# Kernel tuning notes

Hardware: AMD Instinct MI355X
Metric: run time of the kernel (lower is better)

## Reference

```python
import jax, jax.numpy as jnp
import numpy as np

N_NODES = 50000
N_EDGES = 800000
DIM = 128
LN_EPS = 1e-5


def _gcn_conv(x, src, dst, W, b, n_nodes):
    h = x @ W  # [N, D]
    loop = jnp.arange(n_nodes, dtype=src.dtype)
    src_f = jnp.concatenate([src, loop])
    dst_f = jnp.concatenate([dst, loop])
    deg = jax.ops.segment_sum(jnp.ones_like(dst_f, dtype=h.dtype), dst_f,
                              num_segments=n_nodes)  # in-degree incl. self-loop (>=1)
    dinv = jax.lax.rsqrt(deg)
    norm = dinv[src_f] * dinv[dst_f]  # [E+N]
    msg = norm[:, None] * h[src_f]  # gather + scale
    out = jax.ops.segment_sum(msg, dst_f, num_segments=n_nodes)
    return out + b


def _layer_norm(h, w, b):
    mu = jnp.mean(h, axis=-1, keepdims=True)
    var = jnp.mean(jnp.square(h - mu), axis=-1, keepdims=True)
    return (h - mu) * jax.lax.rsqrt(var + LN_EPS) * w + b


def setup_inputs() -> dict:
    key = jax.random.key(0)
    ks = jax.random.split(key, 8)
    x = jax.random.normal(ks[0], (N_NODES, DIM), dtype=jnp.float32)
    edge_index = jax.random.randint(ks[1], (2, N_EDGES), 0, N_NODES, dtype=jnp.int64)
    s = 1.0 / np.sqrt(DIM)
    W0 = jax.random.uniform(ks[2], (DIM, DIM), jnp.float32, -s, s)
    b0 = jnp.zeros((DIM,), jnp.float32)
    W1 = jax.random.uniform(ks[3], (DIM, DIM), jnp.float32, -s, s)
    b1 = jnp.zeros((DIM,), jnp.float32)
    ln0_w = jnp.ones((DIM,), jnp.float32)
    ln0_b = jnp.zeros((DIM,), jnp.float32)
    ln1_w = jnp.ones((DIM,), jnp.float32)
    ln1_b = jnp.zeros((DIM,), jnp.float32)
    return {"x": x, "edge_index": edge_index, "W0": W0, "b0": b0, "W1": W1,
            "b1": b1, "ln0_w": ln0_w, "ln0_b": ln0_b, "ln1_w": ln1_w, "ln1_b": ln1_b}


def reference(x, edge_index, W0, b0, W1, b1, ln0_w, ln0_b, ln1_w, ln1_b):
    src, dst = edge_index[0], edge_index[1]
    n = x.shape[0]
    # layer 0 (dropout is identity in eval mode)
    h = _gcn_conv(x, src, dst, W0, b0, n)
    h = jax.nn.relu(_layer_norm(h, ln0_w, ln0_b)) + x
    # layer 1
    h2 = _gcn_conv(h, src, dst, W1, b1, n)
    h2 = jax.nn.relu(_layer_norm(h2, ln1_w, ln1_b)) + h
    return h2
```

## Files before the change

kernel.cpp:

```cpp
#include <hip/hip_runtime.h>
#include <hip/hip_bf16.h>

#define NDIM 128
#define NNODES 50000
#define CAP 64
#define SWZ(b) ((b) ^ ((((b) >> 8) & 7) << 4))

typedef short bf16x8 __attribute__((ext_vector_type(8)));
typedef float f32x4 __attribute__((ext_vector_type(4)));

__device__ __forceinline__ unsigned short f2bf(float f) {
    unsigned u = __builtin_bit_cast(unsigned, f);
    unsigned r = (u + 0x7FFF + ((u >> 16) & 1)) >> 16;
    return (unsigned short)r;
}
__device__ __forceinline__ float bf2f(unsigned short u) {
    return __builtin_bit_cast(float, (unsigned)u << 16);
}

__device__ __forceinline__ void gl_lds16(const void* g, void* l) {
    __builtin_amdgcn_global_load_lds(
        (const __attribute__((address_space(1))) unsigned int*)g,
        (__attribute__((address_space(3))) unsigned int*)l, 16, 0, 0);
}

__global__ __launch_bounds__(256) void k_build(const int* __restrict__ src,
                                               const int* __restrict__ dst,
                                               int* __restrict__ cnt,
                                               int* __restrict__ bucket, int E) {
    int e = blockIdx.x * 256 + threadIdx.x;
    if (e >= E) return;
    int d = dst[e];
    int p = atomicAdd(&cnt[d], 1);
    if (p < CAP) bucket[(long)d * CAP + p] = src[e];
}

__global__ __launch_bounds__(256) void k_prep(const int* __restrict__ cnt,
                                              float* __restrict__ dinv,
                                              const float* __restrict__ W0,
                                              const float* __restrict__ W1,
                                              unsigned short* __restrict__ Ws0,
                                              unsigned short* __restrict__ Ws1) {
    int b = blockIdx.x;
    if (b < 196) {
        int i = b * 256 + threadIdx.x;
        if (i < NNODES) dinv[i] = rsqrtf((float)cnt[i] + 1.0f);
    } else {
        int t = (b - 196) * 256 + threadIdx.x;
        const float* W = (t >> 14) ? W1 : W0;
        unsigned short* Wd = (t >> 14) ? Ws1 : Ws0;
        int e = t & 16383;
        int k = e >> 7, c = e & 127;
        int byteb = c * 256 + k * 2;
        Wd[SWZ(byteb) >> 1] = f2bf(W[k * NDIM + c]);
    }
}

__global__ __launch_bounds__(256) void k_gemm(const float* __restrict__ X,
                                              const unsigned short* __restrict__ Wsw,
                                              const float* __restrict__ dinv,
                                              unsigned short* __restrict__ Hb,
                                              int n) {
    __shared__ char sW[32768];
    const int wave = threadIdx.x >> 6, lane = threadIdx.x & 63;
    {
        const char* g = (const char*)Wsw;
#pragma unroll
        for (int i = 0; i < 8; i++) {
            int off = (i * 4 + wave) * 1024 + lane * 16;
            gl_lds16(g + off, sW + off);
        }
    }
    const int r16 = lane & 15, hi = lane >> 4;
    const int nodeb = blockIdx.x * 64 + wave * 16;
    int arow = nodeb + r16; if (arow > n - 1) arow = n - 1;

    bf16x8 a[4];
    const float* xp = X + (size_t)arow * NDIM + hi * 8;
#pragma unroll
    for (int kc = 0; kc < 4; kc++) {
        float4 f0 = *(const float4*)(xp + kc * 32);
        float4 f1 = *(const float4*)(xp + kc * 32 + 4);
        bf16x8 v;
        v[0] = f2bf(f0.x); v[1] = f2bf(f0.y); v[2] = f2bf(f0.z); v[3] = f2bf(f0.w);
        v[4] = f2bf(f1.x); v[5] = f2bf(f1.y); v[6] = f2bf(f1.z); v[7] = f2bf(f1.w);
        a[kc] = v;
    }
    float dr[4];
#pragma unroll
    for (int r = 0; r < 4; r++) {
        int row = nodeb + hi * 4 + r;
        dr[r] = dinv[row < n ? row : n - 1];
    }
    __syncthreads();

#pragma unroll
    for (int ct = 0; ct < 8; ct++) {
        f32x4 acc = {0.f, 0.f, 0.f, 0.f};
#pragma unroll
        for (int kc = 0; kc < 4; kc++) {
            int bb = (ct * 16 + r16) * 256 + kc * 64 + hi * 16;
            bf16x8 bw = *(const bf16x8*)(sW + SWZ(bb));
            acc = __builtin_amdgcn_mfma_f32_16x16x32_bf16(a[kc], bw, acc, 0, 0, 0);
        }
#pragma unroll
        for (int r = 0; r < 4; r++) {
            int row = nodeb + hi * 4 + r;
            if (row < n)
                Hb[(size_t)row * NDIM + ct * 16 + r16] = f2bf(acc[r] * dr[r]);
        }
    }
}

__global__ __launch_bounds__(256) void k_agg(const unsigned short* __restrict__ hb,
                                             const float* __restrict__ xres,
                                             const int* __restrict__ bucket,
                                             const int* __restrict__ cnt,
                                             const float* __restrict__ dinv,
                                             const float* __restrict__ bias,
                                             const float* __restrict__ lnw,
                                             const float* __restrict__ lnb,
                                             float* __restrict__ out) {
    const int tid = threadIdx.x;
    const int l16 = tid & 15;
    const int node = blockIdx.x * 16 + (tid >> 4);
    const int d0 = l16 * 8;

    const float dv = dinv[node];
    int c = cnt[node]; if (c > CAP) c = CAP;

    float acc[8];
    {
        bf16x8 sv = *(const bf16x8*)(hb + (size_t)node * NDIM + d0);
#pragma unroll
        for (int t = 0; t < 8; t++) acc[t] = bf2f((unsigned short)sv[t]);
    }

    const int* bk = bucket + (size_t)node * CAP;
    int j = 0;
    for (; j + 4 <= c; j += 4) {
        int s0 = bk[j], s1 = bk[j + 1], s2 = bk[j + 2], s3 = bk[j + 3];
        bf16x8 r0 = *(const bf16x8*)(hb + (size_t)s0 * NDIM + d0);
        bf16x8 r1 = *(const bf16x8*)(hb + (size_t)s1 * NDIM + d0);
        bf16x8 r2 = *(const bf16x8*)(hb + (size_t)s2 * NDIM + d0);
        bf16x8 r3 = *(const bf16x8*)(hb + (size_t)s3 * NDIM + d0);
#pragma unroll
        for (int t = 0; t < 8; t++)
            acc[t] += (bf2f((unsigned short)r0[t]) + bf2f((unsigned short)r1[t]))
                    + (bf2f((unsigned short)r2[t]) + bf2f((unsigned short)r3[t]));
    }
    for (; j < c; j++) {
        int s = bk[j];
        bf16x8 r = *(const bf16x8*)(hb + (size_t)s * NDIM + d0);
#pragma unroll
        for (int t = 0; t < 8; t++) acc[t] += bf2f((unsigned short)r[t]);
    }

    float v[8];
    float4 bb0 = *(const float4*)(bias + d0);
    float4 bb1 = *(const float4*)(bias + d0 + 4);
    v[0] = fmaf(dv, acc[0], bb0.x); v[1] = fmaf(dv, acc[1], bb0.y);
    v[2] = fmaf(dv, acc[2], bb0.z); v[3] = fmaf(dv, acc[3], bb0.w);
    v[4] = fmaf(dv, acc[4], bb1.x); v[5] = fmaf(dv, acc[5], bb1.y);
    v[6] = fmaf(dv, acc[6], bb1.z); v[7] = fmaf(dv, acc[7], bb1.w);

    float s = 0.f;
#pragma unroll
    for (int t = 0; t < 8; t++) s += v[t];
#pragma unroll
    for (int o = 1; o < 16; o <<= 1) s += __shfl_xor(s, o);
    const float mu = s * (1.0f / 128.0f);

    float e[8], q = 0.f;
#pragma unroll
    for (int t = 0; t < 8; t++) { e[t] = v[t] - mu; q += e[t] * e[t]; }
#pragma unroll
    for (int o = 1; o < 16; o <<= 1) q += __shfl_xor(q, o);
    const float rinv = rsqrtf(q * (1.0f / 128.0f) + 1e-5f);

    float4 w0 = *(const float4*)(lnw + d0), w1 = *(const float4*)(lnw + d0 + 4);
    float4 lb0 = *(const float4*)(lnb + d0), lb1 = *(const float4*)(lnb + d0 + 4);
    float4 x0 = *(const float4*)(xres + (size_t)node * NDIM + d0);
    float4 x1 = *(const float4*)(xres + (size_t)node * NDIM + d0 + 4);

    float4 o0, o1;
    o0.x = fmaxf(fmaf(e[0] * rinv, w0.x, lb0.x), 0.f) + x0.x;
    o0.y = fmaxf(fmaf(e[1] * rinv, w0.y, lb0.y), 0.f) + x0.y;
    o0.z = fmaxf(fmaf(e[2] * rinv, w0.z, lb0.z), 0.f) + x0.z;
    o0.w = fmaxf(fmaf(e[3] * rinv, w0.w, lb0.w), 0.f) + x0.w;
    o1.x = fmaxf(fmaf(e[4] * rinv, w1.x, lb1.x), 0.f) + x1.x;
    o1.y = fmaxf(fmaf(e[5] * rinv, w1.y, lb1.y), 0.f) + x1.y;
    o1.z = fmaxf(fmaf(e[6] * rinv, w1.z, lb1.z), 0.f) + x1.z;
    o1.w = fmaxf(fmaf(e[7] * rinv, w1.w, lb1.w), 0.f) + x1.w;
    *(float4*)(out + (size_t)node * NDIM + d0) = o0;
    *(float4*)(out + (size_t)node * NDIM + d0 + 4) = o1;
}

extern "C" void kernel_launch(void* const* d_in, const int* in_sizes, int n_in,
                              void* d_out, int out_size, void* d_ws, size_t ws_size,
                              hipStream_t stream) {
    const float* x    = (const float*)d_in[0];
    const int*   ei   = (const int*)d_in[1];
    const float* W0   = (const float*)d_in[2];
    const float* b0   = (const float*)d_in[3];
    const float* W1   = (const float*)d_in[4];
    const float* b1   = (const float*)d_in[5];
    const float* ln0w = (const float*)d_in[6];
    const float* ln0b = (const float*)d_in[7];
    const float* ln1w = (const float*)d_in[8];
    const float* ln1b = (const float*)d_in[9];
    float* out = (float*)d_out;

    const int E = in_sizes[1] / 2;
    const int* src = ei;
    const int* dst = ei + E;

    char* ws = (char*)d_ws;
    size_t o = 0;
    int*   cnt    = (int*)(ws + o);                 o += (size_t)50048 * 4;
    float* dinv   = (float*)(ws + o);               o += (size_t)50048 * 4;
    int*   bucket = (int*)(ws + o);                 o += (size_t)NNODES * CAP * 4;
    unsigned short* hb = (unsigned short*)(ws + o); o += (size_t)NNODES * NDIM * 2;
    float* xmid   = (float*)(ws + o);               o += (size_t)NNODES * NDIM * 4;
    unsigned short* Ws0 = (unsigned short*)(ws + o); o += (size_t)NDIM * NDIM * 2;
    unsigned short* Ws1 = (unsigned short*)(ws + o); o += (size_t)NDIM * NDIM * 2;

    hipMemsetAsync(cnt, 0, NNODES * sizeof(int), stream);
    k_build<<<(E + 255) / 256, 256, 0, stream>>>(src, dst, cnt, bucket, E);
    k_prep<<<324, 256, 0, stream>>>(cnt, dinv, W0, W1, Ws0, Ws1);

    const int gemm_grid = (NNODES + 63) / 64;
    k_gemm<<<gemm_grid, 256, 0, stream>>>(x, Ws0, dinv, hb, NNODES);
    k_agg<<<NNODES / 16, 256, 0, stream>>>(hb, x, bucket, cnt, dinv, b0,
                                           ln0w, ln0b, xmid);
    k_gemm<<<gemm_grid, 256, 0, stream>>>(xmid, Ws1, dinv, hb, NNODES);
    k_agg<<<NNODES / 16, 256, 0, stream>>>(hb, xmid, bucket, cnt, dinv, b1,
                                           ln1w, ln1b, out);
}
```

Measured before the change: 229.6 us.

## Overlap CSR bucket build with first GEMM in a combined kernel

Merges the edge-bucket build into the first GEMM launch: extra blocks beyond the GEMM grid run the atomic bucket fill while the other blocks compute X·W0. Because the degrees are not known yet, the GEMM writes unscaled bf16 rows, and a new k_scale pass computes dinv and rescales hb afterward. The aim is to hide the atomic-heavy build behind the GEMM and remove one launch. The cost is an extra read-modify-write pass over hb and a second bf16 rounding of the scaled values. Bucket stores also become nontemporal.

```diff
diff --git a/kernel.cpp b/kernel.cpp
--- a/kernel.cpp
+++ b/kernel.cpp
@@ -5,6 +5,8 @@
 #define NNODES 50000
 #define CAP 64
 #define SWZ(b) ((b) ^ ((((b) >> 8) & 7) << 4))
+#define GEMM_GRID 782
+#define BUILD_GRID 2048
 
 typedef short bf16x8 __attribute__((ext_vector_type(8)));
 typedef float f32x4 __attribute__((ext_vector_type(4)));
@@ -24,36 +26,97 @@
         (__attribute__((address_space(3))) unsigned int*)l, 16, 0, 0);
 }
 
-__global__ __launch_bounds__(256) void k_build(const int* __restrict__ src,
-                                               const int* __restrict__ dst,
-                                               int* __restrict__ cnt,
-                                               int* __restrict__ bucket, int E) {
-    int e = blockIdx.x * 256 + threadIdx.x;
-    if (e >= E) return;
-    int d = dst[e];
-    int p = atomicAdd(&cnt[d], 1);
-    if (p < CAP) bucket[(long)d * CAP + p] = src[e];
-}
-
-__global__ __launch_bounds__(256) void k_prep(const int* __restrict__ cnt,
-                                              float* __restrict__ dinv,
-                                              const float* __restrict__ W0,
+__global__ __launch_bounds__(256) void k_prep(const float* __restrict__ W0,
                                               const float* __restrict__ W1,
                                               unsigned short* __restrict__ Ws0,
                                               unsigned short* __restrict__ Ws1) {
-    int b = blockIdx.x;
-    if (b < 196) {
-        int i = b * 256 + threadIdx.x;
-        if (i < NNODES) dinv[i] = rsqrtf((float)cnt[i] + 1.0f);
-    } else {
-        int t = (b - 196) * 256 + threadIdx.x;
-        const float* W = (t >> 14) ? W1 : W0;
-        unsigned short* Wd = (t >> 14) ? Ws1 : Ws0;
-        int e = t & 16383;
-        int k = e >> 7, c = e & 127;
-        int byteb = c * 256 + k * 2;
-        Wd[SWZ(byteb) >> 1] = f2bf(W[k * NDIM + c]);
-    }
+    int t = blockIdx.x * 256 + threadIdx.x;
+    const float* W = (t >> 14) ? W1 : W0;
+    unsigned short* Wd = (t >> 14) ? Ws1 : Ws0;
+    int e = t & 16383;
+    int k = e >> 7, c = e & 127;
+    int byteb = c * 256 + k * 2;
+    Wd[SWZ(byteb) >> 1] = f2bf(W[k * NDIM + c]);
+}
+
+__global__ __launch_bounds__(256) void k_mega(const float* __restrict__ X,
+                                              const unsigned short* __restrict__ Wsw,
+                                              unsigned short* __restrict__ Hb,
+                                              const int* __restrict__ src,
+                                              const int* __restrict__ dst,
+                                              int* __restrict__ cnt,
+                                              int* __restrict__ bucket,
+                                              int E, int n) {
+    __shared__ char sW[32768];
+    if (blockIdx.x >= GEMM_GRID) {
+        int e0 = (blockIdx.x - GEMM_GRID) * 256 + threadIdx.x;
+        for (int e = e0; e < E; e += BUILD_GRID * 256) {
+            int d = dst[e];
+            int p = atomicAdd(&cnt[d], 1);
+            if (p < CAP)
+                __builtin_nontemporal_store(src[e], &bucket[(long)d * CAP + p]);
+        }
+        return;
+    }
+    const int wave = threadIdx.x >> 6, lane = threadIdx.x & 63;
+    {
+        const char* g = (const char*)Wsw;
+#pragma unroll
+        for (int i = 0; i < 8; i++) {
+            int off = (i * 4 + wave) * 1024 + lane * 16;
+            gl_lds16(g + off, sW + off);
+        }
+    }
+    const int r16 = lane & 15, hi = lane >> 4;
+    const int nodeb = blockIdx.x * 64 + wave * 16;
+    int arow = nodeb + r16; if (arow > n - 1) arow = n - 1;
+
+    bf16x8 a[4];
+    const float* xp = X + (size_t)arow * NDIM + hi * 8;
+#pragma unroll
+    for (int kc = 0; kc < 4; kc++) {
+        float4 f0 = *(const float4*)(xp + kc * 32);
+        float4 f1 = *(const float4*)(xp + kc * 32 + 4);
+        bf16x8 v;
+        v[0] = f2bf(f0.x); v[1] = f2bf(f0.y); v[2] = f2bf(f0.z); v[3] = f2bf(f0.w);
+        v[4] = f2bf(f1.x); v[5] = f2bf(f1.y); v[6] = f2bf(f1.z); v[7] = f2bf(f1.w);
+        a[kc] = v;
+    }
+    __syncthreads();
+
+#pragma unroll
+    for (int ct = 0; ct < 8; ct++) {
+        f32x4 acc = {0.f, 0.f, 0.f, 0.f};
+#pragma unroll
+        for (int kc = 0; kc < 4; kc++) {
+            int bb = (ct * 16 + r16) * 256 + kc * 64 + hi * 16;
+            bf16x8 bw = *(const bf16x8*)(sW + SWZ(bb));
+            acc = __builtin_amdgcn_mfma_f32_16x16x32_bf16(a[kc], bw, acc, 0, 0, 0);
+        }
+#pragma unroll
+        for (int r = 0; r < 4; r++) {
+            int row = nodeb + hi * 4 + r;
+            if (row < n)
+                Hb[(size_t)row * NDIM + ct * 16 + r16] = f2bf(acc[r]);
+        }
+    }
+}
+
+__global__ __launch_bounds__(256) void k_scale(unsigned short* __restrict__ hb,
+                                               const int* __restrict__ cnt,
+                                               float* __restrict__ dinv) {
+    const int tid = threadIdx.x;
+    const int l16 = tid & 15;
+    const int row = blockIdx.x * 16 + (tid >> 4);
+    const float dv = rsqrtf((float)cnt[row] + 1.0f);
+    if (l16 == 0) dinv[row] = dv;
+    unsigned short* p = hb + (size_t)row * NDIM + l16 * 8;
+    bf16x8 v = *(const bf16x8*)p;
+    bf16x8 o;
+#pragma unroll
+    for (int t = 0; t < 8; t++)
+        o[t] = (short)f2bf(bf2f((unsigned short)v[t]) * dv);
+    *(bf16x8*)p = o;
 }
 
 __global__ __launch_bounds__(256) void k_gemm(const float* __restrict__ X,
@@ -217,23 +280,23 @@
 
     char* ws = (char*)d_ws;
     size_t o = 0;
-    int*   cnt    = (int*)(ws + o);                 o += (size_t)50048 * 4;
-    float* dinv   = (float*)(ws + o);               o += (size_t)50048 * 4;
-    int*   bucket = (int*)(ws + o);                 o += (size_t)NNODES * CAP * 4;
-    unsigned short* hb = (unsigned short*)(ws + o); o += (size_t)NNODES * NDIM * 2;
-    float* xmid   = (float*)(ws + o);               o += (size_t)NNODES * NDIM * 4;
+    int*   cnt    = (int*)(ws + o);                  o += (size_t)50048 * 4;
+    float* dinv   = (float*)(ws + o);                o += (size_t)50048 * 4;
+    int*   bucket = (int*)(ws + o);                  o += (size_t)NNODES * CAP * 4;
+    unsigned short* hb = (unsigned short*)(ws + o);  o += (size_t)NNODES * NDIM * 2;
+    float* xmid   = (float*)(ws + o);                o += (size_t)NNODES * NDIM * 4;
     unsigned short* Ws0 = (unsigned short*)(ws + o); o += (size_t)NDIM * NDIM * 2;
     unsigned short* Ws1 = (unsigned short*)(ws + o); o += (size_t)NDIM * NDIM * 2;
 
     hipMemsetAsync(cnt, 0, NNODES * sizeof(int), stream);
-    k_build<<<(E + 255) / 256, 256, 0, stream>>>(src, dst, cnt, bucket, E);
-    k_prep<<<324, 256, 0, stream>>>(cnt, dinv, W0, W1, Ws0, Ws1);
-
-    const int gemm_grid = (NNODES + 63) / 64;
-    k_gemm<<<gemm_grid, 256, 0, stream>>>(x, Ws0, dinv, hb, NNODES);
+    k_prep<<<128, 256, 0, stream>>>(W0, W1, Ws0, Ws1);
+
+    k_mega<<<GEMM_GRID + BUILD_GRID, 256, 0, stream>>>(x, Ws0, hb, src, dst,
+                                                       cnt, bucket, E, NNODES);
+    k_scale<<<NNODES / 16, 256, 0, stream>>>(hb, cnt, dinv);
     k_agg<<<NNODES / 16, 256, 0, stream>>>(hb, x, bucket, cnt, dinv, b0,
                                            ln0w, ln0b, xmid);
-    k_gemm<<<gemm_grid, 256, 0, stream>>>(xmid, Ws1, dinv, hb, NNODES);
+    k_gemm<<<GEMM_GRID, 256, 0, stream>>>(xmid, Ws1, dinv, hb, NNODES);
     k_agg<<<NNODES / 16, 256, 0, stream>>>(hb, xmid, bucket, cnt, dinv, b1,
                                            ln1w, ln1b, out);
 }
```

Result: slower. 244.6 us (+6.5%).
